# Performance work log

Hardware: AMD Instinct MI355X
Metric: run time of the kernel (lower is better)

## Reference

```python
import jax, jax.numpy as jnp
import numpy as np

SEQ, BATCH, IN, HID = 2048, 64, 256, 256


def setup_inputs() -> dict:
    key = jax.random.key(0)
    ks = jax.random.split(key, 9)
    s_in = 1.0 / np.sqrt(IN)
    s_h = 1.0 / np.sqrt(HID)
    return {
        "x": jax.random.normal(ks[0], (SEQ, BATCH, IN), dtype=jnp.float32),
        "hidden": jnp.zeros((BATCH, HID), dtype=jnp.float32),
        # torch nn.Linear params: weight (out, in), bias (out,)
        "Wz": jax.random.uniform(ks[1], (HID, IN), jnp.float32, -s_in, s_in),
        "bz": jax.random.uniform(ks[2], (HID,), jnp.float32, -s_in, s_in),
        "Uz": jax.random.uniform(ks[3], (HID, HID), jnp.float32, -s_h, s_h),
        "cz": jax.random.uniform(ks[4], (HID,), jnp.float32, -s_h, s_h),
        "Wh": jax.random.uniform(ks[5], (HID, IN), jnp.float32, -s_in, s_in),
        "bh": jax.random.uniform(ks[6], (HID,), jnp.float32, -s_in, s_in),
        "Uh": jax.random.uniform(ks[7], (HID, HID), jnp.float32, -s_h, s_h),
        "ch": jax.random.uniform(ks[8], (HID,), jnp.float32, -s_h, s_h),
    }


def reference(x, hidden, Wz, bz, Uz, cz, Wh, bh, Uh, ch):
    # Precompute all input projections in two batched GEMMs: (S,B,I)@(I,H)
    xz = jnp.einsum("sbi,hi->sbh", x, Wz) + bz  # W_z x_t + b_z
    xh = jnp.einsum("sbi,hi->sbh", x, Wh) + bh  # W_h x_t + b_h

    def step(h, inp):
        xz_t, xh_t = inp
        z = jax.nn.sigmoid(xz_t + h @ Uz.T + cz)
        h_tilde = jnp.tanh(xh_t + h @ Uh.T + ch)
        h_new = (1.0 - z) * h + z * h_tilde
        return h_new, h_new

    h_final, outputs = jax.lax.scan(step, hidden, (xz, xh))
    return outputs, h_final
```

## Files before the change

kernel.cpp:

```cpp
#include <hip/hip_runtime.h>
#include <math.h>

#define SEQ   2048
#define BATCH 64
#define IN    256
#define HID   256
#define NBLK  (SEQ / 8)

typedef _Float16 hf2 __attribute__((ext_vector_type(2)));
typedef _Float16 hf4 __attribute__((ext_vector_type(4)));
typedef _Float16 hf8 __attribute__((ext_vector_type(8)));
typedef float    f32x2 __attribute__((ext_vector_type(2)));
typedef float    f32x4 __attribute__((ext_vector_type(4)));

static __device__ __forceinline__ float dot2(hf2 a, hf2 b, float c) {
#if __has_builtin(__builtin_amdgcn_fdot2)
    return __builtin_amdgcn_fdot2(a, b, c, false);
#else
    return fmaf((float)a.x, (float)b.x, fmaf((float)a.y, (float)b.y, c));
#endif
}

template <int CTRL>
static __device__ __forceinline__ float dpp_add(float v) {
    const int pv = __builtin_amdgcn_update_dpp(
        0, __builtin_bit_cast(int, v), CTRL, 0xF, 0xF, true);
    return v + __builtin_bit_cast(float, pv);
}

static __device__ __forceinline__ float fast_sigmoid(float x) {
    return __builtin_amdgcn_rcpf(1.0f + __expf(-x));
}

static __device__ __forceinline__ float fast_tanh(float x) {
    const float e = __expf(-2.0f * x);
    return fmaf(2.0f, __builtin_amdgcn_rcpf(1.0f + e), -1.0f);
}

static __device__ __forceinline__ hf8 cvt8(const float4& a, const float4& b) {
    hf8 f;
    f[0] = (_Float16)a.x; f[1] = (_Float16)a.y;
    f[2] = (_Float16)a.z; f[3] = (_Float16)a.w;
    f[4] = (_Float16)b.x; f[5] = (_Float16)b.y;
    f[6] = (_Float16)b.z; f[7] = (_Float16)b.w;
    return f;
}

static __device__ __forceinline__ void bar_lds() {
    asm volatile("s_waitcnt lgkmcnt(0)" ::: "memory");
    __builtin_amdgcn_s_barrier();
}

__global__ __launch_bounds__(256) void w16_kernel(
    const float* __restrict__ Wz, const float* __restrict__ Wh,
    _Float16* __restrict__ W16)
{
    const int idx = blockIdx.x * 256 + threadIdx.x;
    const int row = idx >> 8;
    const int col = idx & 255;
    const float v = (row < 256) ? Wz[row * 256 + col] : Wh[(row - 256) * 256 + col];
    W16[idx] = (_Float16)v;
}

__global__ __launch_bounds__(256) void proj_mfma_kernel(
    const float* __restrict__ x,
    const _Float16* __restrict__ W16,
    const float* __restrict__ bz, const float* __restrict__ cz,
    const float* __restrict__ bh, const float* __restrict__ ch,
    _Float16* __restrict__ xz16,
    float* __restrict__ xh_out)
{
    const int tid  = threadIdx.x;
    const int lane = tid & 63;
    const int w    = tid >> 6;
    const int m0   = blockIdx.x * 16;
    const int col0 = w * 128;

    const int r = lane & 15;
    const int g = lane >> 4;

    f32x4 acc[8] = {f32x4{0,0,0,0}, f32x4{0,0,0,0}, f32x4{0,0,0,0}, f32x4{0,0,0,0},
                    f32x4{0,0,0,0}, f32x4{0,0,0,0}, f32x4{0,0,0,0}, f32x4{0,0,0,0}};

    const float*    xrow  = x   + (size_t)(m0 + r) * IN + g * 8;
    const _Float16* wbase = W16 + (size_t)(col0 + r) * IN + g * 8;

#pragma unroll
    for (int kt = 0; kt < 8; ++kt) {
        const float4 xa = *reinterpret_cast<const float4*>(xrow + kt * 32);
        const float4 xb = *reinterpret_cast<const float4*>(xrow + kt * 32 + 4);
        const hf8 a = cvt8(xa, xb);
#pragma unroll
        for (int t = 0; t < 8; ++t) {
            const hf8 bfrag = *reinterpret_cast<const hf8*>(
                wbase + (size_t)t * 16 * IN + kt * 32);
            acc[t] = __builtin_amdgcn_mfma_f32_16x16x32_f16(a, bfrag, acc[t], 0, 0, 0);
        }
    }

    if (w < 2) {
#pragma unroll
        for (int t = 0; t < 8; ++t) {
            const int c = col0 + t * 16 + r;
            const float bsum = bz[c] + cz[c];
#pragma unroll
            for (int reg = 0; reg < 4; ++reg) {
                const int m = m0 + 4 * g + reg;
                xz16[(size_t)m * HID + c] = (_Float16)(acc[t][reg] + bsum);
            }
        }
    } else {
#pragma unroll
        for (int t = 0; t < 8; ++t) {
            const int c = col0 - 256 + t * 16 + r;
            const float bsum = bh[c] + ch[c];
#pragma unroll
            for (int reg = 0; reg < 4; ++reg) {
                const int m = m0 + 4 * g + reg;
                xh_out[(size_t)m * HID + c] = acc[t][reg] + bsum;
            }
        }
    }
}

__global__ __launch_bounds__(1024, 1) void rec_dot2_kernel(
    const float* __restrict__ hidden0,
    const float* __restrict__ Uz,
    const float* __restrict__ Uh,
    const _Float16* __restrict__ xz16,
    float* __restrict__ out,
    float* __restrict__ h_final)
{
    const int b   = blockIdx.x;
    const int tid = threadIdx.x;
    const int og  = tid >> 2;
    const int q   = tid & 3;

    __shared__ __align__(16) _Float16 hbuf[2][320];
    __shared__ __align__(16) _Float16 xzs[2][8][256];
    __shared__ __align__(16) float    xhs[2][8][256];

    hf2 uz[32], uh[32];
    {
        const float* pz = Uz + (size_t)og * HID + q * 64;
        const float* ph = Uh + (size_t)og * HID + q * 64;
#pragma unroll
        for (int i = 0; i < 16; ++i) {
            float4 v;
            v = *reinterpret_cast<const float4*>(pz + 4 * i);
            uz[2*i]   = hf2{(_Float16)v.x, (_Float16)v.y};
            uz[2*i+1] = hf2{(_Float16)v.z, (_Float16)v.w};
            v = *reinterpret_cast<const float4*>(ph + 4 * i);
            uh[2*i]   = hf2{(_Float16)v.x, (_Float16)v.y};
            uh[2*i+1] = hf2{(_Float16)v.z, (_Float16)v.w};
        }
    }

    if (tid < 256) {
        hbuf[0][tid + (tid >> 5) * 8] = (_Float16)hidden0[b * HID + tid];
    }
    float hp = hidden0[b * HID + og];
    float* pst = out + (size_t)b * HID + og;
    const int og_sk = og + (og >> 5) * 8;

    const int srow = tid >> 7;
    const int scol = (tid & 127) * 2;
    hf2   rz;
    f32x2 rh;
    {
        const size_t a0 = ((size_t)srow * BATCH + b) * HID + scol;
        *reinterpret_cast<hf2*>(&xzs[0][srow][scol]) =
            *reinterpret_cast<const hf2*>(xz16 + a0);
        *reinterpret_cast<f32x2*>(&xhs[0][srow][scol]) =
            *reinterpret_cast<const f32x2*>(out + a0);
        const size_t a1 = ((size_t)(8 + srow) * BATCH + b) * HID + scol;
        rz = *reinterpret_cast<const hf2*>(xz16 + a1);
        rh = *reinterpret_cast<const f32x2*>(out + a1);
    }
    __syncthreads();

    for (int j = 0; j < NBLK; ++j) {
        const int jb = j & 1;
#pragma unroll
        for (int s = 0; s < 8; ++s) {
            const float xzc = (float)xzs[jb][s][og];
            const float xhc = xhs[jb][s][og];
            const _Float16* hsl = &hbuf[s & 1][q * 80];
            float za = 0.f, zb = 0.f, ha = 0.f, hb = 0.f;
#pragma unroll
            for (int c8 = 0; c8 < 8; ++c8) {
                const int off = 8 * c8 + ((c8 >> 2) << 3);
                const hf8 hv = *reinterpret_cast<const hf8*>(hsl + off);
                const hf2 p0 = __builtin_shufflevector(hv, hv, 0, 1);
                const hf2 p1 = __builtin_shufflevector(hv, hv, 2, 3);
                const hf2 p2 = __builtin_shufflevector(hv, hv, 4, 5);
                const hf2 p3 = __builtin_shufflevector(hv, hv, 6, 7);
                if (c8 & 1) {
                    zb = dot2(p0, uz[4*c8+0], zb);
                    zb = dot2(p1, uz[4*c8+1], zb);
                    zb = dot2(p2, uz[4*c8+2], zb);
                    zb = dot2(p3, uz[4*c8+3], zb);
                    hb = dot2(p0, uh[4*c8+0], hb);
                    hb = dot2(p1, uh[4*c8+1], hb);
                    hb = dot2(p2, uh[4*c8+2], hb);
                    hb = dot2(p3, uh[4*c8+3], hb);
                } else {
                    za = dot2(p0, uz[4*c8+0], za);
                    za = dot2(p1, uz[4*c8+1], za);
                    za = dot2(p2, uz[4*c8+2], za);
                    za = dot2(p3, uz[4*c8+3], za);
                    ha = dot2(p0, uh[4*c8+0], ha);
                    ha = dot2(p1, uh[4*c8+1], ha);
                    ha = dot2(p2, uh[4*c8+2], ha);
                    ha = dot2(p3, uh[4*c8+3], ha);
                }
            }
            float accz = za + zb;
            float acch = ha + hb;
            accz = dpp_add<0xB1>(accz);
            acch = dpp_add<0xB1>(acch);
            accz = dpp_add<0x4E>(accz);
            acch = dpp_add<0x4E>(acch);
            const float z  = fast_sigmoid(accz + xzc);
            const float th = fast_tanh(acch + xhc);
            hp = fmaf(z, th - hp, hp);
            if (q == 0) {
                *pst = hp;
                hbuf[(s + 1) & 1][og_sk] = (_Float16)hp;
            }
            pst += (size_t)BATCH * HID;
            if (s == 7 && j + 1 < NBLK) {
                *reinterpret_cast<hf2*>(&xzs[jb ^ 1][srow][scol])   = rz;
                *reinterpret_cast<f32x2*>(&xhs[jb ^ 1][srow][scol]) = rh;
                int trow = 8 * (j + 2) + srow;
                if (trow >= SEQ) trow = SEQ - 1;
                const size_t an = ((size_t)trow * BATCH + b) * HID + scol;
                rz = *reinterpret_cast<const hf2*>(xz16 + an);
                rh = *reinterpret_cast<const f32x2*>(out + an);
            }
            bar_lds();
        }
    }

    if (q == 0) {
        h_final[(size_t)b * HID + og] = hp;
    }
}

extern "C" void kernel_launch(void* const* d_in, const int* in_sizes, int n_in,
                              void* d_out, int out_size, void* d_ws, size_t ws_size,
                              hipStream_t stream) {
    const float* x      = (const float*)d_in[0];
    const float* hidden = (const float*)d_in[1];
    const float* Wz     = (const float*)d_in[2];
    const float* bz     = (const float*)d_in[3];
    const float* Uz     = (const float*)d_in[4];
    const float* cz     = (const float*)d_in[5];
    const float* Wh     = (const float*)d_in[6];
    const float* bh     = (const float*)d_in[7];
    const float* Uh     = (const float*)d_in[8];
    const float* ch     = (const float*)d_in[9];

    float* out     = (float*)d_out;
    float* h_final = out + (size_t)SEQ * BATCH * HID;

    _Float16* xz16 = (_Float16*)d_ws;
    _Float16* W16  = (_Float16*)((char*)d_ws + ((size_t)64 << 20));

    w16_kernel<<<512, 256, 0, stream>>>(Wz, Wh, W16);

    proj_mfma_kernel<<<(SEQ * BATCH) / 16, 256, 0, stream>>>(
        x, W16, bz, cz, bh, ch, xz16, out);

    rec_dot2_kernel<<<BATCH, 1024, 0, stream>>>(
        hidden, Uz, Uh, xz16, out, h_final);
}
```

Measured before the change: 2.052 ms.

## Halve recurrent block size: two threads per hidden unit with wider K slices

The recurrent kernel now runs 512 threads per batch block instead of 1024. Each pair of threads splits one hidden unit's 256-long dot product, so each thread holds 128 columns of Uz/Uh in registers (twice as many). The cross-lane reduction drops to one DPP step, and the per-step barrier spans fewer waves. Staging loads are widened to 4-element vectors. The cost is more serial dot2 work per thread and higher register pressure, which could spill.

```diff
diff --git a/kernel.cpp b/kernel.cpp
--- a/kernel.cpp
+++ b/kernel.cpp
@@ -123,7 +123,7 @@
     }
 }
 
-__global__ __launch_bounds__(1024, 1) void rec_dot2_kernel(
+__global__ __launch_bounds__(512, 2) void rec_dot2_kernel(
     const float* __restrict__ hidden0,
     const float* __restrict__ Uz,
     const float* __restrict__ Uh,
@@ -133,19 +133,19 @@
 {
     const int b   = blockIdx.x;
     const int tid = threadIdx.x;
-    const int og  = tid >> 2;
-    const int q   = tid & 3;
+    const int og  = tid >> 1;
+    const int q   = tid & 1;
 
     __shared__ __align__(16) _Float16 hbuf[2][320];
     __shared__ __align__(16) _Float16 xzs[2][8][256];
     __shared__ __align__(16) float    xhs[2][8][256];
 
-    hf2 uz[32], uh[32];
+    hf2 uz[64], uh[64];
     {
-        const float* pz = Uz + (size_t)og * HID + q * 64;
-        const float* ph = Uh + (size_t)og * HID + q * 64;
-#pragma unroll
-        for (int i = 0; i < 16; ++i) {
+        const float* pz = Uz + (size_t)og * HID + q * 128;
+        const float* ph = Uh + (size_t)og * HID + q * 128;
+#pragma unroll
+        for (int i = 0; i < 32; ++i) {
             float4 v;
             v = *reinterpret_cast<const float4*>(pz + 4 * i);
             uz[2*i]   = hf2{(_Float16)v.x, (_Float16)v.y};
@@ -163,19 +163,19 @@
     float* pst = out + (size_t)b * HID + og;
     const int og_sk = og + (og >> 5) * 8;
 
-    const int srow = tid >> 7;
-    const int scol = (tid & 127) * 2;
-    hf2   rz;
-    f32x2 rh;
+    const int srow = tid >> 6;
+    const int scol = (tid & 63) * 4;
+    hf4   rz;
+    f32x4 rh;
     {
         const size_t a0 = ((size_t)srow * BATCH + b) * HID + scol;
-        *reinterpret_cast<hf2*>(&xzs[0][srow][scol]) =
-            *reinterpret_cast<const hf2*>(xz16 + a0);
-        *reinterpret_cast<f32x2*>(&xhs[0][srow][scol]) =
-            *reinterpret_cast<const f32x2*>(out + a0);
+        *reinterpret_cast<hf4*>(&xzs[0][srow][scol]) =
+            *reinterpret_cast<const hf4*>(xz16 + a0);
+        *reinterpret_cast<f32x4*>(&xhs[0][srow][scol]) =
+            *reinterpret_cast<const f32x4*>(out + a0);
         const size_t a1 = ((size_t)(8 + srow) * BATCH + b) * HID + scol;
-        rz = *reinterpret_cast<const hf2*>(xz16 + a1);
-        rh = *reinterpret_cast<const f32x2*>(out + a1);
+        rz = *reinterpret_cast<const hf4*>(xz16 + a1);
+        rh = *reinterpret_cast<const f32x4*>(out + a1);
     }
     __syncthreads();
 
@@ -185,42 +185,30 @@
         for (int s = 0; s < 8; ++s) {
             const float xzc = (float)xzs[jb][s][og];
             const float xhc = xhs[jb][s][og];
-            const _Float16* hsl = &hbuf[s & 1][q * 80];
-            float za = 0.f, zb = 0.f, ha = 0.f, hb = 0.f;
-#pragma unroll
-            for (int c8 = 0; c8 < 8; ++c8) {
-                const int off = 8 * c8 + ((c8 >> 2) << 3);
+            const _Float16* hsl = &hbuf[s & 1][q * 160];
+            float z0 = 0.f, z1 = 0.f, z2 = 0.f, z3 = 0.f;
+            float h0 = 0.f, h1 = 0.f, h2 = 0.f, h3 = 0.f;
+#pragma unroll
+            for (int i = 0; i < 16; ++i) {
+                const int off = 8 * i + ((i >> 2) << 3);
                 const hf8 hv = *reinterpret_cast<const hf8*>(hsl + off);
                 const hf2 p0 = __builtin_shufflevector(hv, hv, 0, 1);
                 const hf2 p1 = __builtin_shufflevector(hv, hv, 2, 3);
                 const hf2 p2 = __builtin_shufflevector(hv, hv, 4, 5);
                 const hf2 p3 = __builtin_shufflevector(hv, hv, 6, 7);
-                if (c8 & 1) {
-                    zb = dot2(p0, uz[4*c8+0], zb);
-                    zb = dot2(p1, uz[4*c8+1], zb);
-                    zb = dot2(p2, uz[4*c8+2], zb);
-                    zb = dot2(p3, uz[4*c8+3], zb);
-                    hb = dot2(p0, uh[4*c8+0], hb);
-                    hb = dot2(p1, uh[4*c8+1], hb);
-                    hb = dot2(p2, uh[4*c8+2], hb);
-                    hb = dot2(p3, uh[4*c8+3], hb);
-                } else {
-                    za = dot2(p0, uz[4*c8+0], za);
-                    za = dot2(p1, uz[4*c8+1], za);
-                    za = dot2(p2, uz[4*c8+2], za);
-                    za = dot2(p3, uz[4*c8+3], za);
-                    ha = dot2(p0, uh[4*c8+0], ha);
-                    ha = dot2(p1, uh[4*c8+1], ha);
-                    ha = dot2(p2, uh[4*c8+2], ha);
-                    ha = dot2(p3, uh[4*c8+3], ha);
-                }
-            }
-            float accz = za + zb;
-            float acch = ha + hb;
+                z0 = dot2(p0, uz[4*i+0], z0);
+                z1 = dot2(p1, uz[4*i+1], z1);
+                z2 = dot2(p2, uz[4*i+2], z2);
+                z3 = dot2(p3, uz[4*i+3], z3);
+                h0 = dot2(p0, uh[4*i+0], h0);
+                h1 = dot2(p1, uh[4*i+1], h1);
+                h2 = dot2(p2, uh[4*i+2], h2);
+                h3 = dot2(p3, uh[4*i+3], h3);
+            }
+            float accz = (z0 + z1) + (z2 + z3);
+            float acch = (h0 + h1) + (h2 + h3);
             accz = dpp_add<0xB1>(accz);
             acch = dpp_add<0xB1>(acch);
-            accz = dpp_add<0x4E>(accz);
-            acch = dpp_add<0x4E>(acch);
             const float z  = fast_sigmoid(accz + xzc);
             const float th = fast_tanh(acch + xhc);
             hp = fmaf(z, th - hp, hp);
@@ -230,13 +218,13 @@
             }
             pst += (size_t)BATCH * HID;
             if (s == 7 && j + 1 < NBLK) {
-                *reinterpret_cast<hf2*>(&xzs[jb ^ 1][srow][scol])   = rz;
-                *reinterpret_cast<f32x2*>(&xhs[jb ^ 1][srow][scol]) = rh;
+                *reinterpret_cast<hf4*>(&xzs[jb ^ 1][srow][scol])   = rz;
+                *reinterpret_cast<f32x4*>(&xhs[jb ^ 1][srow][scol]) = rh;
                 int trow = 8 * (j + 2) + srow;
                 if (trow >= SEQ) trow = SEQ - 1;
                 const size_t an = ((size_t)trow * BATCH + b) * HID + scol;
-                rz = *reinterpret_cast<const hf2*>(xz16 + an);
-                rh = *reinterpret_cast<const f32x2*>(out + an);
+                rz = *reinterpret_cast<const hf4*>(xz16 + an);
+                rh = *reinterpret_cast<const f32x4*>(out + an);
             }
             bar_lds();
         }
@@ -272,6 +260,6 @@
     proj_mfma_kernel<<<(SEQ * BATCH) / 16, 256, 0, stream>>>(
         x, W16, bz, cz, bh, ch, xz16, out);
 
-    rec_dot2_kernel<<<BATCH, 1024, 0, stream>>>(
+    rec_dot2_kernel<<<BATCH, 512, 0, stream>>>(
         hidden, Uz, Uh, xz16, out, h_final);
 }
```

Measured after the change: 1.909 ms. -7.0%, faster.
